# Kernel tuning notes

Hardware: AMD Instinct MI355X
Metric: run time of the kernel (lower is better)

The kernel has to match this reference:

```python
import jax, jax.numpy as jnp
import numpy as np

B, S, D, H = 4, 2048, 1024, 16
HD = D // H

def setup_inputs() -> dict:
    key = jax.random.key(0)
    ks = jax.random.split(key, 5)
    scale = 1.0 / np.sqrt(D)
    x = jax.random.normal(ks[0], (B, S, D), dtype=jnp.float32)
    w_qkv = jax.random.normal(ks[1], (D, 3 * D), dtype=jnp.float32) * scale
    b_qkv = jax.random.normal(ks[2], (3 * D,), dtype=jnp.float32) * 0.01
    w_proj = jax.random.normal(ks[3], (D, D), dtype=jnp.float32) * scale
    b_proj = jax.random.normal(ks[4], (D,), dtype=jnp.float32) * 0.01
    return {"x": x, "w_qkv": w_qkv, "b_qkv": b_qkv, "w_proj": w_proj, "b_proj": b_proj}

def reference(x, w_qkv, b_qkv, w_proj, b_proj):
    b, s, d = x.shape
    qkv = x @ w_qkv + b_qkv                      # [B,S,3D]
    qkv = qkv.reshape(b, s, 3, H, HD)
    q, k, v = jnp.moveaxis(qkv, 2, 0)            # each [B,S,H,HD]
    q = q.transpose(0, 2, 1, 3)                  # [B,H,S,HD]
    k = k.transpose(0, 2, 1, 3)
    v = v.transpose(0, 2, 1, 3)
    scale = 1.0 / jnp.sqrt(jnp.asarray(HD, dtype=x.dtype))
    scores = jnp.einsum('bhqd,bhkd->bhqk', q, k) * scale
    attn = jax.nn.softmax(scores, axis=-1)
    out = jnp.einsum('bhqk,bhkd->bhqd', attn, v)  # [B,H,S,HD]
    out = out.transpose(0, 2, 1, 3).reshape(b, s, d)
    return out @ w_proj + b_proj
```

## Files before the change

kernel.cpp:

```cpp
#include <hip/hip_runtime.h>

#define B_  4
#define S_  2048
#define D_  1024
#define H_  16
#define HD_ 64
#define M_  (B_*S_)
#define QSCALE 0.1803368801111204f

typedef unsigned short u16;
typedef __bf16 bf16x8 __attribute__((ext_vector_type(8)));
typedef __bf16 bf16x2 __attribute__((ext_vector_type(2)));
typedef float  f32x4  __attribute__((ext_vector_type(4)));
typedef float  f32x16 __attribute__((ext_vector_type(16)));

__device__ __forceinline__ u16 f2bf(float f) {
  unsigned int u = __float_as_uint(f);
  u += 0x7fffu + ((u >> 16) & 1u);
  return (u16)(u >> 16);
}
__device__ __forceinline__ unsigned int packbf2(float lo, float hi) {
#if __has_builtin(__builtin_amdgcn_cvt_pk_bf16_f32)
  union { bf16x2 v; unsigned int u; } c;
  c.v = __builtin_amdgcn_cvt_pk_bf16_f32(lo, hi);
  return c.u;
#else
  return (unsigned int)f2bf(lo) | ((unsigned int)f2bf(hi) << 16);
#endif
}
__device__ __forceinline__ void gld16(const void* g, void* l) {
  __builtin_amdgcn_global_load_lds(
      (const __attribute__((address_space(1))) unsigned int*)g,
      (__attribute__((address_space(3))) unsigned int*)l, 16, 0, 0);
}
#define WAIT_VM3() asm volatile("s_waitcnt vmcnt(3)" ::: "memory")
#define WAIT_VM0() asm volatile("s_waitcnt vmcnt(0)" ::: "memory")
#define MFMA32(a,b,c) __builtin_amdgcn_mfma_f32_32x32x16_bf16(a,b,c,0,0,0)
#define MFMA16(a,b,c) __builtin_amdgcn_mfma_f32_16x16x32_bf16(a,b,c,0,0,0)

__device__ __forceinline__ size_t off16e(int r, int k) {
  return ((size_t)((r >> 7) * 32 + (k >> 5))) * 4096
       + (size_t)((r >> 4) & 7) * 512
       + (size_t)(((k >> 3) & 3) * 16 + (r & 15)) * 8 + (k & 7);
}
__device__ __forceinline__ size_t offA32(int bh, int s, int hd) {
  return ((size_t)(bh * 32 + (s >> 6)) * 8 + ((s >> 5) & 1) * 4 + (hd >> 4)) * 512
       + (size_t)(((hd >> 3) & 1) * 32 + (s & 31)) * 8 + (hd & 7);
}
__device__ __forceinline__ size_t offVT(int bh, int s, int hd) {
  return ((size_t)(bh * 32 + (s >> 6)) * 8 + (hd >> 5) * 4 + ((s >> 4) & 3)) * 512
       + (size_t)(((s >> 3) & 1) * 32 + (hd & 31)) * 8 + (s & 7);
}

__global__ void cvt_f32_bf16(const float* __restrict__ in, u16* __restrict__ out, int n4) {
  int i = blockIdx.x * 256 + threadIdx.x;
  if (i < n4) {
    float4 v = ((const float4*)in)[i];
    int m = i >> 8;
    int k = (i & 255) * 4;
    *(uint2*)&out[off16e(m, k)] = make_uint2(packbf2(v.x, v.y), packbf2(v.z, v.w));
  }
}

__global__ void transpose_w(const float* __restrict__ in, u16* __restrict__ out, int R, int C) {
  __shared__ float tile[32][33];
  int c0 = blockIdx.x * 32, r0 = blockIdx.y * 32;
  int tx = threadIdx.x, ty = threadIdx.y;
  #pragma unroll
  for (int i = 0; i < 4; i++)
    tile[ty + i*8][tx] = in[(size_t)(r0 + ty + i*8) * C + c0 + tx];
  __syncthreads();
  #pragma unroll
  for (int i = 0; i < 4; i++)
    out[off16e(c0 + ty + i*8, r0 + tx)] = f2bf(tile[tx][ty + i*8]);
}

__device__ __forceinline__ void gemm_mainloop(
    const u16* __restrict__ Ab, const u16* __restrict__ Bb0,
    const u16* __restrict__ Bb1, u16* As, u16* Bs,
    f32x4 (&acc)[4][4], const int t, const int w, const int l)
{
  const int wm4 = (w >> 2) * 4;
  const int ct  = (w & 3) >> 1;
  const int wn1 = w & 1;

  #pragma unroll
  for (int kg = 0; kg < 2; ++kg) {
    gld16(Ab  + (size_t)kg * 4096 + t*8, (char*)(As + (0*2 + kg)*4096) + w*1024);
    gld16(Bb0 + (size_t)kg * 4096 + t*8, (char*)(Bs + ((0*2 + 0)*2 + kg)*4096) + w*1024);
    gld16(Bb1 + (size_t)kg * 4096 + t*8, (char*)(Bs + ((0*2 + 1)*2 + kg)*4096) + w*1024);
  }
  WAIT_VM0();
  __syncthreads();

  for (int kt = 0; kt < 16; ++kt) {
    const int cur = kt & 1, nxt = cur ^ 1;
    #pragma unroll
    for (int kk = 0; kk < 2; ++kk) {
      bf16x8 a[4], b[4];
      const u16* Ar = As + (cur*2 + kk)*4096;
      const u16* Br = Bs + ((cur*2 + ct)*2 + kk)*4096;
      #pragma unroll
      for (int mt = 0; mt < 4; ++mt)
        a[mt] = *(const bf16x8*)(Ar + (wm4 + mt)*512 + l*8);
      #pragma unroll
      for (int nt = 0; nt < 4; ++nt)
        b[nt] = *(const bf16x8*)(Br + (wn1*4 + nt)*512 + l*8);

      if (kt < 15) {
        const size_t gs = (size_t)((kt + 1)*2 + kk) * 4096 + t*8;
        gld16(Ab  + gs, (char*)(As + (nxt*2 + kk)*4096) + w*1024);
        gld16(Bb0 + gs, (char*)(Bs + ((nxt*2 + 0)*2 + kk)*4096) + w*1024);
        gld16(Bb1 + gs, (char*)(Bs + ((nxt*2 + 1)*2 + kk)*4096) + w*1024);
      }

      __builtin_amdgcn_s_barrier();
      asm volatile("s_waitcnt lgkmcnt(0)" ::: "memory");
      __builtin_amdgcn_s_setprio(1);
      #pragma unroll
      for (int mt = 0; mt < 4; ++mt)
        #pragma unroll
        for (int nt = 0; nt < 4; ++nt)
          acc[mt][nt] = MFMA16(a[mt], b[nt], acc[mt][nt]);
      __builtin_amdgcn_s_setprio(0);

      if (kt < 15)      { WAIT_VM3(); }
      else if (kk == 0) { WAIT_VM0(); }
      __builtin_amdgcn_s_barrier();
    }
  }
}

__global__ __launch_bounds__(512,2) void gemm_qkv(
    const u16* __restrict__ X, const u16* __restrict__ WT,
    const float* __restrict__ bias,
    u16* __restrict__ qb, u16* __restrict__ kb, u16* __restrict__ vb)
{
  __shared__ u16 As[2*2*4096];
  __shared__ u16 Bs[2*2*2*4096];
  const int t = threadIdx.x, w = t >> 6, l = t & 63;
  const int m0 = blockIdx.y * 128, n0 = blockIdx.x * 256;
  const u16* Ab  = X  + (size_t)blockIdx.y * 32 * 4096;
  const u16* Bb0 = WT + (size_t)(2*blockIdx.x + 0) * 32 * 4096;
  const u16* Bb1 = WT + (size_t)(2*blockIdx.x + 1) * 32 * 4096;

  f32x4 acc[4][4] = {};
  gemm_mainloop(Ab, Bb0, Bb1, As, Bs, acc, t, w, l);

  const int wm = (w >> 2) * 64, wn = (w & 3) * 64, lr = l & 15, quad = l >> 4;
  #pragma unroll
  for (int mt = 0; mt < 4; mt++)
  #pragma unroll
  for (int nt = 0; nt < 4; nt++) {
    int n = n0 + wn + nt * 16 + lr;
    float bia = bias[n];
    int which = n >> 10, hh = (n >> 6) & 15, hd = n & 63;
    #pragma unroll
    for (int r = 0; r < 4; r++) {
      int m = m0 + wm + mt * 16 + quad * 4 + r;
      float v = acc[mt][nt][r] + bia;
      int bb = m >> 11, s = m & 2047, bh = bb * 16 + hh;
      if (which == 0)      qb[offA32(bh, s, hd)] = f2bf(v * QSCALE);
      else if (which == 1) kb[offA32(bh, s, hd)] = f2bf(v);
      else                 vb[offVT(bh, s, hd)] = f2bf(v);
    }
  }
}

__global__ __launch_bounds__(512,2) void gemm_proj(
    const u16* __restrict__ X, const u16* __restrict__ WT,
    const float* __restrict__ bias, float* __restrict__ out)
{
  __shared__ u16 As[2*2*4096];
  __shared__ u16 Bs[2*2*2*4096];
  const int t = threadIdx.x, w = t >> 6, l = t & 63;
  const int m0 = blockIdx.y * 128, n0 = blockIdx.x * 256;
  const u16* Ab  = X  + (size_t)blockIdx.y * 32 * 4096;
  const u16* Bb0 = WT + (size_t)(2*blockIdx.x + 0) * 32 * 4096;
  const u16* Bb1 = WT + (size_t)(2*blockIdx.x + 1) * 32 * 4096;

  f32x4 acc[4][4] = {};
  gemm_mainloop(Ab, Bb0, Bb1, As, Bs, acc, t, w, l);

  const int wm = (w >> 2) * 64, wn = (w & 3) * 64, lr = l & 15, quad = l >> 4;
  #pragma unroll
  for (int mt = 0; mt < 4; mt++)
  #pragma unroll
  for (int nt = 0; nt < 4; nt++) {
    int n = n0 + wn + nt * 16 + lr;
    float bia = bias[n];
    #pragma unroll
    for (int r = 0; r < 4; r++) {
      int m = m0 + wm + mt * 16 + quad * 4 + r;
      out[(size_t)m * D_ + n] = acc[mt][nt][r] + bia;
    }
  }
}

__global__ __launch_bounds__(256,4) void attn(
    const u16* __restrict__ qb, const u16* __restrict__ kb,
    const u16* __restrict__ vt, u16* __restrict__ ob)
{
  __shared__ u16 Ks[2][8*512];
  __shared__ u16 Vs[2][8*512];
  const int t = threadIdx.x, w = t >> 6, l = t & 63, l31 = l & 31, h = l >> 5;
  const int i = blockIdx.x, xcd = i & 7, j = i >> 3;
  const int bh = xcd * 8 + (j >> 4), qt = j & 15;
  const int b = bh >> 4, hh = bh & 15;
  const int s0 = qt * 128 + w * 32;
  const u16* qp = qb + (size_t)bh * 131072;
  const u16* kp = kb + (size_t)bh * 131072;
  const u16* vp = vt + (size_t)bh * 131072;

  bf16x8 qa[4];
  {
    const size_t qbase = ((size_t)(qt*2 + (w >> 1)) * 8 + (w & 1) * 4) * 512;
    #pragma unroll
    for (int kk = 0; kk < 4; kk++)
      qa[kk] = *(const bf16x8*)(qp + qbase + (size_t)kk * 512 + l*8);
  }

  union { unsigned int u[4]; bf16x8 v; } ones;
  ones.u[0] = ones.u[1] = ones.u[2] = ones.u[3] = 0x3F803F80u;

  f32x16 o[2] = {};
  f32x16 lacc = {};

  #pragma unroll
  for (int c = 0; c < 2; c++) {
    gld16(kp + (size_t)(w*2 + c) * 512 + l*8, (char*)&Ks[0][0] + (w*2 + c)*1024);
    gld16(vp + (size_t)(w*2 + c) * 512 + l*8, (char*)&Vs[0][0] + (w*2 + c)*1024);
  }
  WAIT_VM0();
  __syncthreads();

  for (int kt = 0; kt < 32; kt++) {
    const int cur = kt & 1, nxt = cur ^ 1;
    const u16* Kb = &Ks[cur][0];
    const u16* Vb = &Vs[cur][0];

    if (kt < 31) {
      const size_t gs = (size_t)(kt + 1) * 4096;
      #pragma unroll
      for (int c = 0; c < 2; c++) {
        gld16(kp + gs + (size_t)(w*2 + c) * 512 + l*8, (char*)&Ks[nxt][0] + (w*2 + c)*1024);
        gld16(vp + gs + (size_t)(w*2 + c) * 512 + l*8, (char*)&Vs[nxt][0] + (w*2 + c)*1024);
      }
    }

    f32x16 sf[2] = {};
    #pragma unroll
    for (int kk = 0; kk < 4; kk++) {
      bf16x8 ka0 = *(const bf16x8*)(Kb + (0*4 + kk)*512 + l*8);
      bf16x8 ka1 = *(const bf16x8*)(Kb + (1*4 + kk)*512 + l*8);
      sf[0] = MFMA32(ka0, qa[kk], sf[0]);
      sf[1] = MFMA32(ka1, qa[kk], sf[1]);
    }

    unsigned int pk[2][4][2];
    #pragma unroll
    for (int mt = 0; mt < 2; mt++)
      #pragma unroll
      for (int e = 0; e < 4; e++) {
        float p0 = __builtin_amdgcn_exp2f(sf[mt][4*e+0]);
        float p1 = __builtin_amdgcn_exp2f(sf[mt][4*e+1]);
        float p2 = __builtin_amdgcn_exp2f(sf[mt][4*e+2]);
        float p3 = __builtin_amdgcn_exp2f(sf[mt][4*e+3]);
        pk[mt][e][0] = packbf2(p0, p1);
        pk[mt][e][1] = packbf2(p2, p3);
      }

    #pragma unroll
    for (int kk2 = 0; kk2 < 4; kk2++) {
      const int mt = kk2 >> 1, k1 = kk2 & 1;
      bf16x8 bv0 = *(const bf16x8*)(Vb + (0*4 + kk2)*512 + l*8);
      bf16x8 bv1 = *(const bf16x8*)(Vb + (1*4 + kk2)*512 + l*8);
      union { unsigned int u[4]; bf16x8 v; } pa;
#if __has_builtin(__builtin_amdgcn_permlane32_swap)
      auto s02 = __builtin_amdgcn_permlane32_swap(pk[mt][2*k1][0], pk[mt][2*k1+1][0], false, false);
      auto s13 = __builtin_amdgcn_permlane32_swap(pk[mt][2*k1][1], pk[mt][2*k1+1][1], false, false);
      pa.u[0] = s02[0]; pa.u[1] = s13[0]; pa.u[2] = s02[1]; pa.u[3] = s13[1];
#else
      unsigned int s0_ = h ? pk[mt][2*k1][0] : pk[mt][2*k1+1][0];
      unsigned int s1_ = h ? pk[mt][2*k1][1] : pk[mt][2*k1+1][1];
      unsigned int r0 = (unsigned int)__shfl_xor((int)s0_, 32);
      unsigned int r1 = (unsigned int)__shfl_xor((int)s1_, 32);
      pa.u[0] = h ? r0 : pk[mt][2*k1][0];
      pa.u[1] = h ? r1 : pk[mt][2*k1][1];
      pa.u[2] = h ? pk[mt][2*k1+1][0] : r0;
      pa.u[3] = h ? pk[mt][2*k1+1][1] : r1;
#endif
      o[0] = MFMA32(pa.v, bv0, o[0]);
      o[1] = MFMA32(pa.v, bv1, o[1]);
      lacc = MFMA32(pa.v, ones.v, lacc);
    }

    if (kt < 31) {
      WAIT_VM0();
      __syncthreads();
    }
  }

  #pragma unroll
  for (int rb = 0; rb < 4; rb++) {
    #pragma unroll
    for (int c = 0; c < 4; c++) {
      int r = rb*4 + c;
      float iv = 1.f / lacc[r];
      int row = s0 + c + 8*rb + 4*h;
      int m = b * S_ + row;
      int d0 = hh*64 + l31, d1 = hh*64 + 32 + l31;
      ob[off16e(m, d0)] = f2bf(o[0][r] * iv);
      ob[off16e(m, d1)] = f2bf(o[1][r] * iv);
    }
  }
}

extern "C" void kernel_launch(void* const* d_in, const int* in_sizes, int n_in,
                              void* d_out, int out_size, void* d_ws, size_t ws_size,
                              hipStream_t stream) {
  const float* x      = (const float*)d_in[0];
  const float* w_qkv  = (const float*)d_in[1];
  const float* b_qkv  = (const float*)d_in[2];
  const float* w_proj = (const float*)d_in[3];
  const float* b_proj = (const float*)d_in[4];
  float* out = (float*)d_out;

  char* ws = (char*)d_ws;
  u16* xbf    = (u16*)ws; ws += (size_t)M_ * D_ * 2;
  u16* wqkvT  = (u16*)ws; ws += (size_t)3 * D_ * D_ * 2;
  u16* wprojT = (u16*)ws; ws += (size_t)D_ * D_ * 2;
  u16* qbuf   = (u16*)ws; ws += (size_t)M_ * D_ * 2;
  u16* kbuf   = (u16*)ws; ws += (size_t)M_ * D_ * 2;
  u16* vtbuf  = (u16*)ws; ws += (size_t)M_ * D_ * 2;
  u16* aobuf  = (u16*)ws; ws += (size_t)M_ * D_ * 2;

  cvt_f32_bf16<<<(M_ * D_ / 4 + 255) / 256, 256, 0, stream>>>(x, xbf, M_ * D_ / 4);
  transpose_w<<<dim3(3 * D_ / 32, D_ / 32), dim3(32, 8), 0, stream>>>(w_qkv, wqkvT, D_, 3 * D_);
  transpose_w<<<dim3(D_ / 32, D_ / 32), dim3(32, 8), 0, stream>>>(w_proj, wprojT, D_, D_);
  gemm_qkv<<<dim3(3 * D_ / 256, M_ / 128), 512, 0, stream>>>(xbf, wqkvT, b_qkv, qbuf, kbuf, vtbuf);
  attn<<<1024, 256, 0, stream>>>(qbuf, kbuf, vtbuf, aobuf);
  gemm_proj<<<dim3(D_ / 256, M_ / 128), 512, 0, stream>>>(aobuf, wprojT, b_proj, out);
}
```

Baseline: 301.7 us.

## Enlarge GEMM tiles to 256x256 with quadrant-staged pipeline and XCD-aware block mapping

Both projection GEMMs move from 128x256 to 256x256 output tiles. Each K-step is split into four quadrant MFMA phases, and the loads of the next A/B halves are interleaved between those phases with deeper vmcnt waits. Block indices are remapped so neighbouring M tiles share an XCD, which is meant to improve L2 reuse of the X rows. This doubles LDS use and accumulator registers per block and halves the grid, so occupancy and wave count drop, especially for gemm_proj with only 128 blocks.

```diff
diff --git a/kernel.cpp b/kernel.cpp
--- a/kernel.cpp
+++ b/kernel.cpp
@@ -33,8 +33,9 @@
       (const __attribute__((address_space(1))) unsigned int*)g,
       (__attribute__((address_space(3))) unsigned int*)l, 16, 0, 0);
 }
-#define WAIT_VM3() asm volatile("s_waitcnt vmcnt(3)" ::: "memory")
+#define WAIT_VM6() asm volatile("s_waitcnt vmcnt(6)" ::: "memory")
 #define WAIT_VM0() asm volatile("s_waitcnt vmcnt(0)" ::: "memory")
+#define LGKM0()    asm volatile("s_waitcnt lgkmcnt(0)" ::: "memory")
 #define MFMA32(a,b,c) __builtin_amdgcn_mfma_f32_32x32x16_bf16(a,b,c,0,0,0)
 #define MFMA16(a,b,c) __builtin_amdgcn_mfma_f32_16x16x32_bf16(a,b,c,0,0,0)
 
@@ -75,59 +76,109 @@
     out[off16e(c0 + ty + i*8, r0 + tx)] = f2bf(tile[tx][ty + i*8]);
 }
 
-__device__ __forceinline__ void gemm_mainloop(
-    const u16* __restrict__ Ab, const u16* __restrict__ Bb0,
-    const u16* __restrict__ Bb1, u16* As, u16* Bs,
-    f32x4 (&acc)[4][4], const int t, const int w, const int l)
+#define STAGE_A(h, tau, dbuf) \
+  { const u16* s_ = Asrc[h] + (size_t)(2*(tau))*4096 + t*8; \
+    char* d_ = (char*)(As + (((dbuf)*2 + (h))*2)*4096) + w*1024; \
+    gld16(s_, d_); gld16(s_ + 4096, d_ + 8192); }
+#define STAGE_B(h, tau, dbuf) \
+  { const u16* s_ = Bsrc[h] + (size_t)(2*(tau))*4096 + t*8; \
+    char* d_ = (char*)(Bs + (((dbuf)*2 + (h))*2)*4096) + w*1024; \
+    gld16(s_, d_); gld16(s_ + 4096, d_ + 8192); }
+
+__device__ __forceinline__ void gemm_mainloop256(
+    const u16* const Asrc[2], const u16* const Bsrc[2],
+    u16* As, u16* Bs, f32x4 (&acc)[2][2][4][2],
+    const int t, const int w, const int l)
 {
-  const int wm4 = (w >> 2) * 4;
-  const int ct  = (w & 3) >> 1;
-  const int wn1 = w & 1;
-
-  #pragma unroll
-  for (int kg = 0; kg < 2; ++kg) {
-    gld16(Ab  + (size_t)kg * 4096 + t*8, (char*)(As + (0*2 + kg)*4096) + w*1024);
-    gld16(Bb0 + (size_t)kg * 4096 + t*8, (char*)(Bs + ((0*2 + 0)*2 + kg)*4096) + w*1024);
-    gld16(Bb1 + (size_t)kg * 4096 + t*8, (char*)(Bs + ((0*2 + 1)*2 + kg)*4096) + w*1024);
-  }
-  WAIT_VM0();
-  __syncthreads();
-
+  const int frA = (w >> 2) * 4;
+  const int frB = (w & 3) * 2;
+
+  STAGE_A(0, 0, 0); STAGE_B(0, 0, 0); STAGE_B(1, 0, 0); STAGE_A(1, 0, 0);
+  STAGE_A(0, 1, 1); STAGE_B(0, 1, 1); STAGE_B(1, 1, 1);
+  WAIT_VM6();
+  __builtin_amdgcn_s_barrier();
+
+  bf16x8 aR[2][4], b0R[2][2], b1R[2][2];
   for (int kt = 0; kt < 16; ++kt) {
-    const int cur = kt & 1, nxt = cur ^ 1;
+    const int bu = kt & 1, nb = bu ^ 1;
+    const u16* Abuf = As + (bu*2)*2*4096;
+    const u16* Bbuf = Bs + (bu*2)*2*4096;
+
     #pragma unroll
     for (int kk = 0; kk < 2; ++kk) {
-      bf16x8 a[4], b[4];
-      const u16* Ar = As + (cur*2 + kk)*4096;
-      const u16* Br = Bs + ((cur*2 + ct)*2 + kk)*4096;
       #pragma unroll
       for (int mt = 0; mt < 4; ++mt)
-        a[mt] = *(const bf16x8*)(Ar + (wm4 + mt)*512 + l*8);
-      #pragma unroll
-      for (int nt = 0; nt < 4; ++nt)
-        b[nt] = *(const bf16x8*)(Br + (wn1*4 + nt)*512 + l*8);
-
-      if (kt < 15) {
-        const size_t gs = (size_t)((kt + 1)*2 + kk) * 4096 + t*8;
-        gld16(Ab  + gs, (char*)(As + (nxt*2 + kk)*4096) + w*1024);
-        gld16(Bb0 + gs, (char*)(Bs + ((nxt*2 + 0)*2 + kk)*4096) + w*1024);
-        gld16(Bb1 + gs, (char*)(Bs + ((nxt*2 + 1)*2 + kk)*4096) + w*1024);
-      }
-
-      __builtin_amdgcn_s_barrier();
-      asm volatile("s_waitcnt lgkmcnt(0)" ::: "memory");
-      __builtin_amdgcn_s_setprio(1);
+        aR[kk][mt] = *(const bf16x8*)(Abuf + (0*2 + kk)*4096 + (frA + mt)*512 + l*8);
+      #pragma unroll
+      for (int nt = 0; nt < 2; ++nt)
+        b0R[kk][nt] = *(const bf16x8*)(Bbuf + (0*2 + kk)*4096 + (frB + nt)*512 + l*8);
+    }
+    if (kt < 15) STAGE_A(1, kt+1, nb);
+    __builtin_amdgcn_s_barrier();
+    LGKM0();
+    __builtin_amdgcn_s_setprio(1);
+    #pragma unroll
+    for (int mt = 0; mt < 4; ++mt)
+      #pragma unroll
+      for (int nt = 0; nt < 2; ++nt)
+        #pragma unroll
+        for (int kk = 0; kk < 2; ++kk)
+          acc[0][0][mt][nt] = MFMA16(aR[kk][mt], b0R[kk][nt], acc[0][0][mt][nt]);
+    __builtin_amdgcn_s_setprio(0);
+    __builtin_amdgcn_s_barrier();
+
+    #pragma unroll
+    for (int kk = 0; kk < 2; ++kk)
+      #pragma unroll
+      for (int nt = 0; nt < 2; ++nt)
+        b1R[kk][nt] = *(const bf16x8*)(Bbuf + (1*2 + kk)*4096 + (frB + nt)*512 + l*8);
+    if (kt < 14) STAGE_A(0, kt+2, bu);
+    __builtin_amdgcn_s_barrier();
+    LGKM0();
+    __builtin_amdgcn_s_setprio(1);
+    #pragma unroll
+    for (int mt = 0; mt < 4; ++mt)
+      #pragma unroll
+      for (int nt = 0; nt < 2; ++nt)
+        #pragma unroll
+        for (int kk = 0; kk < 2; ++kk)
+          acc[0][1][mt][nt] = MFMA16(aR[kk][mt], b1R[kk][nt], acc[0][1][mt][nt]);
+    __builtin_amdgcn_s_setprio(0);
+    __builtin_amdgcn_s_barrier();
+
+    #pragma unroll
+    for (int kk = 0; kk < 2; ++kk)
       #pragma unroll
       for (int mt = 0; mt < 4; ++mt)
+        aR[kk][mt] = *(const bf16x8*)(Abuf + (1*2 + kk)*4096 + (frA + mt)*512 + l*8);
+    if (kt < 14) STAGE_B(0, kt+2, bu);
+    __builtin_amdgcn_s_barrier();
+    LGKM0();
+    __builtin_amdgcn_s_setprio(1);
+    #pragma unroll
+    for (int mt = 0; mt < 4; ++mt)
+      #pragma unroll
+      for (int nt = 0; nt < 2; ++nt)
         #pragma unroll
-        for (int nt = 0; nt < 4; ++nt)
-          acc[mt][nt] = MFMA16(a[mt], b[nt], acc[mt][nt]);
-      __builtin_amdgcn_s_setprio(0);
-
-      if (kt < 15)      { WAIT_VM3(); }
-      else if (kk == 0) { WAIT_VM0(); }
-      __builtin_amdgcn_s_barrier();
-    }
+        for (int kk = 0; kk < 2; ++kk)
+          acc[1][0][mt][nt] = MFMA16(aR[kk][mt], b0R[kk][nt], acc[1][0][mt][nt]);
+    __builtin_amdgcn_s_setprio(0);
+    __builtin_amdgcn_s_barrier();
+
+    if (kt < 14) STAGE_B(1, kt+2, bu);
+    __builtin_amdgcn_s_barrier();
+    __builtin_amdgcn_s_setprio(1);
+    #pragma unroll
+    for (int mt = 0; mt < 4; ++mt)
+      #pragma unroll
+      for (int nt = 0; nt < 2; ++nt)
+        #pragma unroll
+        for (int kk = 0; kk < 2; ++kk)
+          acc[1][1][mt][nt] = MFMA16(aR[kk][mt], b1R[kk][nt], acc[1][1][mt][nt]);
+    __builtin_amdgcn_s_setprio(0);
+    if (kt <= 13)      { WAIT_VM6(); }
+    else if (kt == 14) { WAIT_VM0(); }
+    __builtin_amdgcn_s_barrier();
   }
 }
 
@@ -136,29 +187,38 @@
     const float* __restrict__ bias,
     u16* __restrict__ qb, u16* __restrict__ kb, u16* __restrict__ vb)
 {
-  __shared__ u16 As[2*2*4096];
+  __shared__ u16 As[2*2*2*4096];
   __shared__ u16 Bs[2*2*2*4096];
   const int t = threadIdx.x, w = t >> 6, l = t & 63;
-  const int m0 = blockIdx.y * 128, n0 = blockIdx.x * 256;
-  const u16* Ab  = X  + (size_t)blockIdx.y * 32 * 4096;
-  const u16* Bb0 = WT + (size_t)(2*blockIdx.x + 0) * 32 * 4096;
-  const u16* Bb1 = WT + (size_t)(2*blockIdx.x + 1) * 32 * 4096;
-
-  f32x4 acc[4][4] = {};
-  gemm_mainloop(Ab, Bb0, Bb1, As, Bs, acc, t, w, l);
-
-  const int wm = (w >> 2) * 64, wn = (w & 3) * 64, lr = l & 15, quad = l >> 4;
+  const int i = blockIdx.x, xcd = i & 7, j = i >> 3;
+  const int byi = xcd * 4 + (j & 3);
+  const int bxi = j >> 2;
+  const int m0 = byi * 256, n0 = bxi * 256;
+  const u16* Asrc[2] = { X  + (size_t)(2*byi + 0)*32*4096,
+                         X  + (size_t)(2*byi + 1)*32*4096 };
+  const u16* Bsrc[2] = { WT + (size_t)(2*bxi + 0)*32*4096,
+                         WT + (size_t)(2*bxi + 1)*32*4096 };
+
+  f32x4 acc[2][2][4][2] = {};
+  gemm_mainloop256(Asrc, Bsrc, As, Bs, acc, t, w, l);
+
+  const int lr = l & 15, quad = l >> 4;
+  const int wr = (w >> 2) * 64, wc = (w & 3) * 32;
+  #pragma unroll
+  for (int MH = 0; MH < 2; MH++)
+  #pragma unroll
+  for (int NH = 0; NH < 2; NH++)
   #pragma unroll
   for (int mt = 0; mt < 4; mt++)
   #pragma unroll
-  for (int nt = 0; nt < 4; nt++) {
-    int n = n0 + wn + nt * 16 + lr;
+  for (int nt = 0; nt < 2; nt++) {
+    int n = n0 + NH*128 + wc + nt*16 + lr;
     float bia = bias[n];
     int which = n >> 10, hh = (n >> 6) & 15, hd = n & 63;
     #pragma unroll
     for (int r = 0; r < 4; r++) {
-      int m = m0 + wm + mt * 16 + quad * 4 + r;
-      float v = acc[mt][nt][r] + bia;
+      int m = m0 + MH*128 + wr + mt*16 + quad*4 + r;
+      float v = acc[MH][NH][mt][nt][r] + bia;
       int bb = m >> 11, s = m & 2047, bh = bb * 16 + hh;
       if (which == 0)      qb[offA32(bh, s, hd)] = f2bf(v * QSCALE);
       else if (which == 1) kb[offA32(bh, s, hd)] = f2bf(v);
@@ -171,28 +231,37 @@
     const u16* __restrict__ X, const u16* __restrict__ WT,
     const float* __restrict__ bias, float* __restrict__ out)
 {
-  __shared__ u16 As[2*2*4096];
+  __shared__ u16 As[2*2*2*4096];
   __shared__ u16 Bs[2*2*2*4096];
   const int t = threadIdx.x, w = t >> 6, l = t & 63;
-  const int m0 = blockIdx.y * 128, n0 = blockIdx.x * 256;
-  const u16* Ab  = X  + (size_t)blockIdx.y * 32 * 4096;
-  const u16* Bb0 = WT + (size_t)(2*blockIdx.x + 0) * 32 * 4096;
-  const u16* Bb1 = WT + (size_t)(2*blockIdx.x + 1) * 32 * 4096;
-
-  f32x4 acc[4][4] = {};
-  gemm_mainloop(Ab, Bb0, Bb1, As, Bs, acc, t, w, l);
-
-  const int wm = (w >> 2) * 64, wn = (w & 3) * 64, lr = l & 15, quad = l >> 4;
+  const int i = blockIdx.x, xcd = i & 7, j = i >> 3;
+  const int byi = xcd * 4 + (j & 3);
+  const int bxi = j >> 2;
+  const int m0 = byi * 256, n0 = bxi * 256;
+  const u16* Asrc[2] = { X  + (size_t)(2*byi + 0)*32*4096,
+                         X  + (size_t)(2*byi + 1)*32*4096 };
+  const u16* Bsrc[2] = { WT + (size_t)(2*bxi + 0)*32*4096,
+                         WT + (size_t)(2*bxi + 1)*32*4096 };
+
+  f32x4 acc[2][2][4][2] = {};
+  gemm_mainloop256(Asrc, Bsrc, As, Bs, acc, t, w, l);
+
+  const int lr = l & 15, quad = l >> 4;
+  const int wr = (w >> 2) * 64, wc = (w & 3) * 32;
+  #pragma unroll
+  for (int MH = 0; MH < 2; MH++)
+  #pragma unroll
+  for (int NH = 0; NH < 2; NH++)
   #pragma unroll
   for (int mt = 0; mt < 4; mt++)
   #pragma unroll
-  for (int nt = 0; nt < 4; nt++) {
-    int n = n0 + wn + nt * 16 + lr;
+  for (int nt = 0; nt < 2; nt++) {
+    int n = n0 + NH*128 + wc + nt*16 + lr;
     float bia = bias[n];
     #pragma unroll
     for (int r = 0; r < 4; r++) {
-      int m = m0 + wm + mt * 16 + quad * 4 + r;
-      out[(size_t)m * D_ + n] = acc[mt][nt][r] + bia;
+      int m = m0 + MH*128 + wr + mt*16 + quad*4 + r;
+      out[(size_t)m * D_ + n] = acc[MH][NH][mt][nt][r] + bia;
     }
   }
 }
@@ -338,7 +407,7 @@
   cvt_f32_bf16<<<(M_ * D_ / 4 + 255) / 256, 256, 0, stream>>>(x, xbf, M_ * D_ / 4);
   transpose_w<<<dim3(3 * D_ / 32, D_ / 32), dim3(32, 8), 0, stream>>>(w_qkv, wqkvT, D_, 3 * D_);
   transpose_w<<<dim3(D_ / 32, D_ / 32), dim3(32, 8), 0, stream>>>(w_proj, wprojT, D_, D_);
-  gemm_qkv<<<dim3(3 * D_ / 256, M_ / 128), 512, 0, stream>>>(xbf, wqkvT, b_qkv, qbuf, kbuf, vtbuf);
+  gemm_qkv<<<384, 512, 0, stream>>>(xbf, wqkvT, b_qkv, qbuf, kbuf, vtbuf);
   attn<<<1024, 256, 0, stream>>>(qbuf, kbuf, vtbuf, aobuf);
-  gemm_proj<<<dim3(D_ / 256, M_ / 128), 512, 0, stream>>>(aobuf, wprojT, b_proj, out);
-}
+  gemm_proj<<<128, 512, 0, stream>>>(aobuf, wprojT, b_proj, out);
+}
```

New measurement: 307.9 us. +2.1%, slower.
